# Kernel tuning notes

Measured on AMD Instinct MI355X. Metric: run time of the kernel, lower is better.

The kernel has to match this reference:

```python
import jax, jax.numpy as jnp
import numpy as np

D_HIDDEN = 1024
NUM_HEADS = 16
D_HEAD = D_HIDDEN // NUM_HEADS


def setup_inputs() -> dict:
    key = jax.random.key(0)
    ks = jax.random.split(key, 9)
    N, S, D = 4, 2048, D_HIDDEN
    s = 1.0 / np.sqrt(D)
    inp = {
        "x": jax.random.normal(ks[0], (N, S, D), dtype=jnp.float32),
        "Wq": jax.random.uniform(ks[1], (D, D), jnp.float32, -s, s),
        "bq": jnp.zeros((D,), jnp.float32),
        "Wk": jax.random.uniform(ks[2], (D, D), jnp.float32, -s, s),
        "bk": jnp.zeros((D,), jnp.float32),
        "Wv": jax.random.uniform(ks[3], (D, D), jnp.float32, -s, s),
        "bv": jnp.zeros((D,), jnp.float32),
        "Wo": jax.random.uniform(ks[4], (D, D), jnp.float32, -s, s),
        "bo": jnp.zeros((D,), jnp.float32),
        "ln_gamma": jnp.ones((D,), jnp.float32),
        "ln_beta": jnp.zeros((D,), jnp.float32),
    }
    return inp


def _layer_norm(x, gamma, beta, eps=1e-5):
    mu = jnp.mean(x, axis=-1, keepdims=True)
    var = jnp.var(x, axis=-1, keepdims=True)
    return (x - mu) * jax.lax.rsqrt(var + eps) * gamma + beta


def reference(x, Wq, bq, Wk, bk, Wv, bv, Wo, bo, ln_gamma, ln_beta):
    N, S, D = x.shape
    H, Dh = NUM_HEADS, D_HEAD
    xn = _layer_norm(x, ln_gamma, ln_beta)
    # torch Linear: y = x @ W.T + b
    q = (xn @ Wq.T + bq).reshape(N, S, H, Dh)
    k = (xn @ Wk.T + bk).reshape(N, S, H, Dh)
    v = (xn @ Wv.T + bv).reshape(N, S, H, Dh)
    # scores: [N, H, S, S]
    scores = jnp.einsum('nxhd,nyhd->nhxy', q, k) / np.sqrt(Dh)
    # causal mask: positions y > x get -inf
    mask = jnp.triu(jnp.full((S, S), -jnp.inf, dtype=scores.dtype), k=1)
    attn = jax.nn.softmax(scores + mask[None, None], axis=-1)
    z = jnp.einsum('nhxy,nyhd->nxhd', attn, v).reshape(N, S, D)
    return z @ Wo.T + bo
```

## Files before the change

kernel.cpp:

```cpp
#include <hip/hip_runtime.h>

typedef unsigned short u16;
typedef unsigned int   u32;
typedef __bf16 bf16x8 __attribute__((ext_vector_type(8)));
typedef float  f32x4  __attribute__((ext_vector_type(4)));
typedef unsigned short u16x8 __attribute__((ext_vector_type(8)));
typedef unsigned short u16x4 __attribute__((ext_vector_type(4)));

#define SEQ 2048
#define DM  1024
#define TOKS 8388608
#define SCLQ 0.18033688f

__device__ __forceinline__ float bf2f(u16 u) {
    u32 i = ((u32)u) << 16;
    float f; __builtin_memcpy(&f, &i, 4); return f;
}
__device__ __forceinline__ u16 f2bf(float f) {
    u32 i; __builtin_memcpy(&i, &f, 4);
    return (u16)((i + 0x7FFFu + ((i >> 16) & 1u)) >> 16);
}
__device__ __forceinline__ bf16x8 ld8(const u16* p) {
    return __builtin_bit_cast(bf16x8, *(const u16x8*)p);
}
#define GLD16(src, dst) __builtin_amdgcn_global_load_lds( \
    (const __attribute__((address_space(1))) void*)(src), \
    (__attribute__((address_space(3))) void*)(dst), 16, 0, 0)

#define SBAR() do { asm volatile("" ::: "memory"); __builtin_amdgcn_sched_barrier(0); \
    __builtin_amdgcn_s_barrier(); __builtin_amdgcn_sched_barrier(0); asm volatile("" ::: "memory"); } while (0)
#define WVM(n) asm volatile("s_waitcnt vmcnt(" #n ")" ::: "memory")

__global__ __launch_bounds__(64) void detect_k(const u32* __restrict__ x, int* __restrict__ flag) {
    const int lane = threadIdx.x;
    u32 w = x[lane];
    int e0 = (int)((w >> 7) & 0xFFu);
    int cnt = (e0 >= 100 && e0 <= 140) ? 1 : 0;
#pragma unroll
    for (int off = 32; off; off >>= 1) cnt += __shfl_xor(cnt, off);
    if (lane == 0) *flag = (cnt < 32) ? 1 : 0;
}

__global__ __launch_bounds__(256) void convert_k(const void* s0, const void* s1, const void* s2, const void* s3,
                                                 const void* v0, const void* v1, const void* v2, const void* v3,
                                                 const void* v4, const void* v5,
                                                 u16* __restrict__ dstW, u16* __restrict__ dstV,
                                                 const int* __restrict__ flagp) {
    const int y = blockIdx.y, tid = threadIdx.x;
    const int fp32m = *flagp;
    const void* src; u16* dst; size_t off;
    if (y < 4) {
        src = (y == 0) ? s0 : (y == 1) ? s1 : (y == 2) ? s2 : s3;
        dst = dstW + (size_t)y * 1048576;
        off = (size_t)blockIdx.x * 1024 + tid * 4;
    } else {
        const int i = blockIdx.x;
        if (i >= 6) return;
        src = (i == 0) ? v0 : (i == 1) ? v1 : (i == 2) ? v2 : (i == 3) ? v3 : (i == 4) ? v4 : v5;
        dst = dstV + (size_t)i * 1024;
        off = (size_t)tid * 4;
    }
    u16x4 o;
    if (fp32m) {
        const float* f = (const float*)src + off;
#pragma unroll
        for (int j = 0; j < 4; ++j) o[j] = f2bf(f[j]);
    } else {
        o = *(const u16x4*)((const u16*)src + off);
    }
    *(u16x4*)(dst + off) = o;
}

__global__ __launch_bounds__(256) void ln_k(const void* __restrict__ xv,
                                            const u16* __restrict__ g,
                                            const u16* __restrict__ b,
                                            u16* __restrict__ xn,
                                            const int* __restrict__ flagp) {
    const int row = blockIdx.x, tid = threadIdx.x;
    const int fp32m = *flagp;
    float f[4], s1 = 0.f, s2 = 0.f;
    if (fp32m) {
        f32x4 v = *(const f32x4*)((const float*)xv + (size_t)row * DM + tid * 4);
#pragma unroll
        for (int j = 0; j < 4; ++j) f[j] = v[j];
    } else {
        u16x4 v = *(const u16x4*)((const u16*)xv + (size_t)row * DM + tid * 4);
#pragma unroll
        for (int j = 0; j < 4; ++j) f[j] = bf2f(v[j]);
    }
#pragma unroll
    for (int j = 0; j < 4; ++j) { s1 += f[j]; s2 += f[j] * f[j]; }
#pragma unroll
    for (int off = 32; off; off >>= 1) { s1 += __shfl_xor(s1, off); s2 += __shfl_xor(s2, off); }
    __shared__ float red[8];
    const int wave = tid >> 6, lane = tid & 63;
    if (lane == 0) { red[wave] = s1; red[4 + wave] = s2; }
    __syncthreads();
    s1 = red[0] + red[1] + red[2] + red[3];
    s2 = red[4] + red[5] + red[6] + red[7];
    const float mu = s1 * (1.f / DM);
    const float var = s2 * (1.f / DM) - mu * mu;
    const float rs = rsqrtf(var + 1e-5f);
    u16x4 gv = *(const u16x4*)(g + tid * 4);
    u16x4 bv = *(const u16x4*)(b + tid * 4);
    u16x4 o;
#pragma unroll
    for (int j = 0; j < 4; ++j) o[j] = f2bf((f[j] - mu) * rs * bf2f(gv[j]) + bf2f(bv[j]));
    *(u16x4*)(xn + (size_t)row * DM + tid * 4) = o;
}

__global__ __launch_bounds__(512, 2) void gemm_qkv_k(const u16* __restrict__ xn, const u16* __restrict__ Wc,
                                                     const u16* __restrict__ Vc,
                                                     u16* __restrict__ Q, u16* __restrict__ K, u16* __restrict__ Vt) {
    __shared__ alignas(16) u16 lds[65536];
    const int tid = threadIdx.x;
    const int w = tid >> 6, lane = tid & 63;
    const int l4 = lane & 15, q4 = lane >> 4;
    const int orig = blockIdx.y * 32 + blockIdx.x;
    const int s = (orig & 7) * 48 + (orig >> 3);
    const int bm = s / 12, bn = s % 12;
    const int wm0 = (w >> 2) * 128, wn = (w & 3) * 64;

    const int srowl = lane >> 2;
    const int schk = (lane & 3) ^ ((lane >> 3) & 3);
    const u16* aS = xn + ((size_t)(bm * 256) + srowl) * DM + schk * 8;
    const u16* bS = Wc + ((size_t)(bn * 256) + srowl) * DM + schk * 8;
    const int rb = w * 16;

    auto STG = [&](int h, int kt, int bq) {
        const size_t kk = (size_t)kt * 32;
        u16* d = lds + bq * 16384;
        if (h == 0)      GLD16(aS + (size_t)rb * DM + kk,         d + rb * 32);
        else if (h == 3) GLD16(aS + (size_t)(128 + rb) * DM + kk, d + 4096 + rb * 32);
        else if (h == 1) GLD16(bS + (size_t)rb * DM + kk,         d + 8192 + rb * 32);
        else             GLD16(bS + (size_t)(128 + rb) * DM + kk, d + 12288 + rb * 32);
    };

    const int swz = (q4 ^ ((l4 >> 1) & 3)) << 3;

    f32x4 acc[8][4] = {};
    bf16x8 af[4], bfv[4];

#pragma unroll
    for (int p = 0; p < 3; ++p) {
        STG(0, p, p); STG(1, p, p); STG(2, p, p); STG(3, p, p);
    }

    for (int kt = 0; kt < 32; ++kt) {
        if (kt <= 29)      { WVM(8); }
        else if (kt == 30) { WVM(4); }
        else               { WVM(0); }
        SBAR();
        const u16* bp = lds + (kt & 3) * 16384;
        const bool pf = (kt < 29);
        const int nb = (kt + 3) & 3;
        if (pf) { STG(0, kt + 3, nb); STG(1, kt + 3, nb); }
#pragma unroll
        for (int mt = 0; mt < 4; ++mt) af[mt] = ld8(bp + (wm0 + mt * 16 + l4) * 32 + swz);
#pragma unroll
        for (int nt = 0; nt < 4; ++nt) bfv[nt] = ld8(bp + 8192 + (wn + nt * 16 + l4) * 32 + swz);
        __builtin_amdgcn_s_setprio(1);
#pragma unroll
        for (int mt = 0; mt < 4; ++mt)
#pragma unroll
            for (int nt = 0; nt < 4; ++nt)
                acc[mt][nt] = __builtin_amdgcn_mfma_f32_16x16x32_bf16(af[mt], bfv[nt], acc[mt][nt], 0, 0, 0);
        __builtin_amdgcn_s_setprio(0);
        if (pf) { STG(2, kt + 3, nb); STG(3, kt + 3, nb); }
#pragma unroll
        for (int mt = 0; mt < 4; ++mt) af[mt] = ld8(bp + (wm0 + 64 + mt * 16 + l4) * 32 + swz);
        __builtin_amdgcn_s_setprio(1);
#pragma unroll
        for (int mt = 0; mt < 4; ++mt)
#pragma unroll
            for (int nt = 0; nt < 4; ++nt)
                acc[mt + 4][nt] = __builtin_amdgcn_mfma_f32_16x16x32_bf16(af[mt], bfv[nt], acc[mt + 4][nt], 0, 0, 0);
        __builtin_amdgcn_s_setprio(0);
    }

    const int whichB = bn >> 2;
    const int cb = (bn & 3) * 256 + wn;
    u16* outp = (whichB == 0) ? Q : (whichB == 1) ? K : Vt;
    const float scl = (whichB == 0) ? SCLQ : 1.0f;
    float bs4[4];
#pragma unroll
    for (int nt = 0; nt < 4; ++nt) bs4[nt] = bf2f(Vc[whichB * 1024 + cb + nt * 16 + l4]);
    if (whichB < 2) {
#pragma unroll
        for (int mt = 0; mt < 8; ++mt) {
            const int row0 = bm * 256 + wm0 + mt * 16 + q4 * 4;
#pragma unroll
            for (int r = 0; r < 4; ++r) {
                u16* rowp = outp + (size_t)(row0 + r) * DM + cb;
#pragma unroll
                for (int nt = 0; nt < 4; ++nt)
                    rowp[nt * 16 + l4] = f2bf((acc[mt][nt][r] + bs4[nt]) * scl);
            }
        }
    } else {
#pragma unroll
        for (int nt = 0; nt < 4; ++nt) {
            const int cc = cb + nt * 16 + l4;
#pragma unroll
            for (int mt = 0; mt < 8; ++mt) {
                const int row0 = bm * 256 + wm0 + mt * 16 + q4 * 4;
                const int nbk = row0 >> 11, s0 = row0 & 2047;
                u16x4 pk;
#pragma unroll
                for (int r = 0; r < 4; ++r) pk[r] = f2bf(acc[mt][nt][r] + bs4[nt]);
                *(u16x4*)(outp + ((size_t)(nbk * 1024 + cc)) * SEQ + s0) = pk;
            }
        }
    }
}

#define LDS_U16 73728

__device__ __forceinline__ void wait_vm12() { asm volatile("s_waitcnt vmcnt(12)" ::: "memory"); }
__device__ __forceinline__ void wait_vm6()  { asm volatile("s_waitcnt vmcnt(6)"  ::: "memory"); }
__device__ __forceinline__ void wait_vm0()  { asm volatile("s_waitcnt vmcnt(0)"  ::: "memory"); }

__device__ __forceinline__ void gemm256x128_out(u16* lds,
                                                const u16* __restrict__ A,
                                                const u16* __restrict__ W,
                                                const u16* __restrict__ bias,
                                                u16* __restrict__ o0,
                                                int fp32m) {
    const int tid = threadIdx.x;
    const int w = tid >> 6, lane = tid & 63;
    const int l4 = lane & 15, q4 = lane >> 4;
    const int bm = blockIdx.x, bn = blockIdx.y;
    const int wm = (w >> 1) * 64, wn = (w & 1) * 64;

    const int srow = lane >> 3;
    const int schk = (lane & 7) ^ srow;
    const u16* sA = A + ((size_t)(bm * 256 + w * 32 + srow)) * DM + (schk << 3);
    const u16* sB = W + ((size_t)(bn * 128 + w * 16 + srow)) * DM + (schk << 3);

    int offA[4][2], offB[4][2];
#pragma unroll
    for (int mt = 0; mt < 4; ++mt)
#pragma unroll
        for (int s = 0; s < 2; ++s) {
            const int row = wm + mt * 16 + l4;
            offA[mt][s] = row * 64 + (((s * 4 + q4) ^ (l4 & 7)) << 3);
        }
#pragma unroll
    for (int nt = 0; nt < 4; ++nt)
#pragma unroll
        for (int s = 0; s < 2; ++s) {
            const int row = wn + nt * 16 + l4;
            offB[nt][s] = 16384 + row * 64 + (((s * 4 + q4) ^ (l4 & 7)) << 3);
        }

    auto STAGE = [&](int kt, int b) {
        const u16* a0 = sA + kt * 64;
        const u16* b0 = sB + kt * 64;
        u16* la = lds + b * 24576 + w * 2048;
        u16* lb = lds + b * 24576 + 16384 + w * 1024;
        GLD16(a0,           la);
        GLD16(a0 + 8 * DM,  la + 512);
        GLD16(a0 + 16 * DM, la + 1024);
        GLD16(a0 + 24 * DM, la + 1536);
        GLD16(b0,           lb);
        GLD16(b0 + 8 * DM,  lb + 512);
    };

    f32x4 acc[4][4] = {};

    STAGE(0, 0); STAGE(1, 1); STAGE(2, 2);

#pragma unroll
    for (int kt = 0; kt < 16; ++kt) {
        const int b = kt % 3;
        if (kt < 14)      wait_vm12();
        else if (kt == 14) wait_vm6();
        else               wait_vm0();
        __builtin_amdgcn_s_barrier();
        __builtin_amdgcn_sched_barrier(0);
        const u16* base = lds + b * 24576;
        bf16x8 af[4][2], bfr[4][2];
#pragma unroll
        for (int mt = 0; mt < 4; ++mt)
#pragma unroll
            for (int s = 0; s < 2; ++s) af[mt][s] = ld8(base + offA[mt][s]);
#pragma unroll
        for (int nt = 0; nt < 2; ++nt)
#pragma unroll
            for (int s = 0; s < 2; ++s) bfr[nt][s] = ld8(base + offB[nt][s]);
        __builtin_amdgcn_s_setprio(1);
#pragma unroll
        for (int mt = 0; mt < 4; ++mt)
#pragma unroll
            for (int nt = 0; nt < 2; ++nt)
#pragma unroll
                for (int s = 0; s < 2; ++s)
                    acc[mt][nt] = __builtin_amdgcn_mfma_f32_16x16x32_bf16(af[mt][s], bfr[nt][s], acc[mt][nt], 0, 0, 0);
        __builtin_amdgcn_s_setprio(0);
#pragma unroll
        for (int nt = 2; nt < 4; ++nt)
#pragma unroll
            for (int s = 0; s < 2; ++s) bfr[nt][s] = ld8(base + offB[nt][s]);
        __builtin_amdgcn_s_setprio(1);
#pragma unroll
        for (int mt = 0; mt < 4; ++mt)
#pragma unroll
            for (int nt = 2; nt < 4; ++nt)
#pragma unroll
                for (int s = 0; s < 2; ++s)
                    acc[mt][nt] = __builtin_amdgcn_mfma_f32_16x16x32_bf16(af[mt][s], bfr[nt][s], acc[mt][nt], 0, 0, 0);
        __builtin_amdgcn_s_setprio(0);
        __builtin_amdgcn_s_barrier();
        __builtin_amdgcn_sched_barrier(0);
        if (kt < 13) STAGE(kt + 3, b);
    }

#pragma unroll
    for (int nt = 0; nt < 4; ++nt) {
        const int cc = bn * 128 + wn + nt * 16 + l4;
        const float bs = bf2f(bias[cc]);
#pragma unroll
        for (int mt = 0; mt < 4; ++mt) {
            const int row0 = bm * 256 + wm + mt * 16 + q4 * 4;
            if (fp32m) {
#pragma unroll
                for (int r = 0; r < 4; ++r)
                    ((float*)o0)[(size_t)(row0 + r) * DM + cc] = acc[mt][nt][r] + bs;
            } else {
#pragma unroll
                for (int r = 0; r < 4; ++r)
                    o0[(size_t)(row0 + r) * DM + cc] = f2bf(acc[mt][nt][r] + bs);
            }
        }
    }
}

__global__ __launch_bounds__(512, 2) void gemm_out_k(const u16* __restrict__ Z, const u16* __restrict__ Wc,
                                                     const u16* __restrict__ Vc,
                                                     u16* __restrict__ out, const int* __restrict__ flagp) {
    __shared__ alignas(16) u16 lds[LDS_U16];
    const int fp32m = *flagp;
    gemm256x128_out(lds, Z, Wc + 3 * 1048576, Vc + 3 * 1024, out, fp32m);
}

__global__ __launch_bounds__(256, 4) void flash_k(const u16* __restrict__ Q,
                                                  const u16* __restrict__ K,
                                                  const u16* __restrict__ Vt,
                                                  u16* __restrict__ Z) {
    const int bh = blockIdx.x;
    const int qb = 15 - (int)blockIdx.y;
    const int n = bh >> 4, h = bh & 15;
    const int tid = threadIdx.x, wave = tid >> 6, lane = tid & 63;
    const int l4 = lane & 15, q4 = lane >> 4;

    __shared__ alignas(16) u16 Ks[2][64 * 32];
    __shared__ alignas(16) u16 Vs[2][64 * 32];
    __shared__ alignas(16) u16 Pl[4][2][16 * 72];

    const int Q0w = qb * 128 + wave * 32;
    bf16x8 qf[2][2];
#pragma unroll
    for (int qt = 0; qt < 2; ++qt) {
        const u16* Qr = Q + ((size_t)(n * SEQ + Q0w + qt * 16 + l4)) * DM + h * 64 + q4 * 8;
        qf[qt][0] = ld8(Qr);
        qf[qt][1] = ld8(Qr + 32);
    }

    const int srow = lane >> 2, scol = (lane & 3) * 8;
    const u16* Kg = K + ((size_t)(n * SEQ + wave * 16 + srow)) * DM + h * 64 + scol;
    const u16* Vg = Vt + ((size_t)(n * 1024 + h * 64 + wave * 16 + srow)) * SEQ + scol;
    u16* KsD0 = &Ks[0][wave * 512];
    u16* KsD1 = &Ks[1][wave * 512];
    u16* VsD0 = &Vs[0][wave * 512];
    u16* VsD1 = &Vs[1][wave * 512];

    f32x4 o[2][4] = {};
    float l_acc[2] = {0.f, 0.f};
    const int nch = 2 * qb + 2;

    for (int c = 0; c < nch; ++c) {
        const int kv0 = c * 64;
        const size_t krow = (size_t)kv0 * DM;
        GLD16(Kg + krow, KsD0);
        GLD16(Kg + krow + 32, KsD1);
        GLD16(Vg + kv0, VsD0);
        GLD16(Vg + kv0 + 32, VsD1);
        __syncthreads();

        bf16x8 a[4][2];
#pragma unroll
        for (int mt = 0; mt < 4; ++mt) {
            a[mt][0] = ld8(&Ks[0][(mt * 16 + l4) * 32 + q4 * 8]);
            a[mt][1] = ld8(&Ks[1][(mt * 16 + l4) * 32 + q4 * 8]);
        }
#pragma unroll
        for (int qt = 0; qt < 2; ++qt) {
            f32x4 st[4];
#pragma unroll
            for (int mt = 0; mt < 4; ++mt) {
                f32x4 zz = {0.f, 0.f, 0.f, 0.f};
                st[mt] = __builtin_amdgcn_mfma_f32_16x16x32_bf16(a[mt][0], qf[qt][0], zz, 0, 0, 0);
                st[mt] = __builtin_amdgcn_mfma_f32_16x16x32_bf16(a[mt][1], qf[qt][1], st[mt], 0, 0, 0);
            }
            const int qg = Q0w + qt * 16 + l4;
            u16* P = Pl[wave][qt];
            float la = l_acc[qt];
#pragma unroll
            for (int mt = 0; mt < 4; ++mt) {
                __bf16 pk[4];
#pragma unroll
                for (int r = 0; r < 4; ++r) {
                    const int kv = kv0 + mt * 16 + q4 * 4 + r;
                    float p = __builtin_amdgcn_exp2f(st[mt][r]);
                    p = (kv > qg) ? 0.f : p;
                    la += p;
                    pk[r] = (__bf16)p;
                }
                *(u16x4*)(P + l4 * 72 + mt * 16 + q4 * 4) = *(u16x4*)pk;
            }
            l_acc[qt] = la;
        }
#pragma unroll
        for (int ks = 0; ks < 2; ++ks) {
            bf16x8 pf0 = ld8(&Pl[wave][0][l4 * 72 + ks * 32 + q4 * 8]);
            bf16x8 pf1 = ld8(&Pl[wave][1][l4 * 72 + ks * 32 + q4 * 8]);
#pragma unroll
            for (int nt = 0; nt < 4; ++nt) {
                bf16x8 vf = ld8(&Vs[ks][(nt * 16 + l4) * 32 + q4 * 8]);
                o[0][nt] = __builtin_amdgcn_mfma_f32_16x16x32_bf16(pf0, vf, o[0][nt], 0, 0, 0);
                o[1][nt] = __builtin_amdgcn_mfma_f32_16x16x32_bf16(pf1, vf, o[1][nt], 0, 0, 0);
            }
        }
        __syncthreads();
    }

#pragma unroll
    for (int qt = 0; qt < 2; ++qt) {
        float l = l_acc[qt];
        l += __shfl_xor(l, 16);
        l += __shfl_xor(l, 32);
        float lr[4];
#pragma unroll
        for (int r = 0; r < 4; ++r) lr[r] = 1.f / __shfl(l, q4 * 4 + r);
#pragma unroll
        for (int nt = 0; nt < 4; ++nt) {
            const int col = h * 64 + nt * 16 + l4;
#pragma unroll
            for (int r = 0; r < 4; ++r) {
                const int row = n * SEQ + Q0w + qt * 16 + q4 * 4 + r;
                Z[(size_t)row * DM + col] = f2bf(o[qt][nt][r] * lr[r]);
            }
        }
    }
}

extern "C" void kernel_launch(void* const* d_in, const int* in_sizes, int n_in,
                              void* d_out, int out_size, void* d_ws, size_t ws_size,
                              hipStream_t stream) {
    const void* x  = d_in[0];
    const void* Wq = d_in[1];
    const void* bq = d_in[2];
    const void* Wk = d_in[3];
    const void* bk = d_in[4];
    const void* Wv = d_in[5];
    const void* bv = d_in[6];
    const void* Wo = d_in[7];
    const void* bo = d_in[8];
    const void* g  = d_in[9];
    const void* b  = d_in[10];
    u16* ws = (u16*)d_ws;

    u16* xn  = ws;
    u16* Qb  = ws + (size_t)TOKS;
    u16* Kb  = ws + (size_t)2 * TOKS;
    u16* Vtb = ws + (size_t)3 * TOKS;
    u16* Zb  = ws;
    u16* Wc  = ws + (size_t)4 * TOKS;
    u16* Vc  = Wc + 4 * 1048576;
    int* flagp = (int*)(Vc + 8 * 1024);

    detect_k<<<dim3(1), 64, 0, stream>>>((const u32*)x, flagp);
    convert_k<<<dim3(1024, 5), 256, 0, stream>>>(Wq, Wk, Wv, Wo, bq, bk, bv, bo, g, b, Wc, Vc, flagp);
    ln_k<<<dim3(4 * SEQ), 256, 0, stream>>>(x, Vc + 4 * 1024, Vc + 5 * 1024, xn, flagp);
    gemm_qkv_k<<<dim3(32, 12), 512, 0, stream>>>(xn, Wc, Vc, Qb, Kb, Vtb);
    flash_k<<<dim3(64, 16), 256, 0, stream>>>(Qb, Kb, Vtb, Zb);
    gemm_out_k<<<dim3(32, 8), 512, 0, stream>>>(Zb, Wc, Vc, (u16*)d_out, flagp);
}
```

Before: 253.1 us.

## Restructure QKV GEMM into a 64-wide K tile with four-phase ping-pong pipeline

Rewrites the QKV projection GEMM main loop to stage 64-wide K slices split by A/B half-tiles into double-buffered LDS slots. Each iteration runs four MFMA phases, with global-to-LDS loads issued between them and explicit lgkmcnt/vmcnt waits plus barriers. The LDS swizzle is changed to an 8-chunk XOR to match the wider rows. The XCD-aware block remapping is dropped in favor of direct blockIdx mapping, which may change L2 locality. A separate GEMM loop goes from full unrolling to unroll 4.

```diff
diff --git a/kernel.cpp b/kernel.cpp
--- a/kernel.cpp
+++ b/kernel.cpp
@@ -30,6 +30,8 @@
 #define SBAR() do { asm volatile("" ::: "memory"); __builtin_amdgcn_sched_barrier(0); \
     __builtin_amdgcn_s_barrier(); __builtin_amdgcn_sched_barrier(0); asm volatile("" ::: "memory"); } while (0)
 #define WVM(n) asm volatile("s_waitcnt vmcnt(" #n ")" ::: "memory")
+#define LGKM0() do { asm volatile("s_waitcnt lgkmcnt(0)" ::: "memory"); \
+    __builtin_amdgcn_sched_barrier(0); } while (0)
 
 __global__ __launch_bounds__(64) void detect_k(const u32* __restrict__ x, int* __restrict__ flag) {
     const int lane = threadIdx.x;
@@ -116,66 +118,101 @@
     const int tid = threadIdx.x;
     const int w = tid >> 6, lane = tid & 63;
     const int l4 = lane & 15, q4 = lane >> 4;
-    const int orig = blockIdx.y * 32 + blockIdx.x;
-    const int s = (orig & 7) * 48 + (orig >> 3);
-    const int bm = s / 12, bn = s % 12;
+    const int bm = blockIdx.x, bn = blockIdx.y;
     const int wm0 = (w >> 2) * 128, wn = (w & 3) * 64;
 
-    const int srowl = lane >> 2;
-    const int schk = (lane & 3) ^ ((lane >> 3) & 3);
-    const u16* aS = xn + ((size_t)(bm * 256) + srowl) * DM + schk * 8;
-    const u16* bS = Wc + ((size_t)(bn * 256) + srowl) * DM + schk * 8;
+    const int srow = lane >> 3, schk = (lane & 7) ^ srow;
+    const u16* aS = xn + ((size_t)(bm * 256) + srow) * DM + schk * 8;
+    const u16* bS = Wc + ((size_t)(bn * 256) + srow) * DM + schk * 8;
     const int rb = w * 16;
 
-    auto STG = [&](int h, int kt, int bq) {
-        const size_t kk = (size_t)kt * 32;
-        u16* d = lds + bq * 16384;
-        if (h == 0)      GLD16(aS + (size_t)rb * DM + kk,         d + rb * 32);
-        else if (h == 3) GLD16(aS + (size_t)(128 + rb) * DM + kk, d + 4096 + rb * 32);
-        else if (h == 1) GLD16(bS + (size_t)rb * DM + kk,         d + 8192 + rb * 32);
-        else             GLD16(bS + (size_t)(128 + rb) * DM + kk, d + 12288 + rb * 32);
+    auto STG = [&](int kind, int ut) {
+        const int slotb = kind * 16384 + (ut & 1) * 8192;
+        int g0;
+        if (kind == 0)      g0 = (rb < 64) ? rb : rb + 64;
+        else if (kind == 1) g0 = (rb < 64) ? rb + 64 : rb + 128;
+        else if (kind == 2) g0 = rb;
+        else                g0 = rb + 128;
+        const u16* src = (kind < 2 ? aS : bS) + (size_t)g0 * DM + (size_t)ut * 64;
+        u16* dst = lds + slotb + rb * 64;
+        GLD16(src, dst);
+        GLD16(src + 8 * DM, dst + 512);
     };
 
-    const int swz = (q4 ^ ((l4 >> 1) & 3)) << 3;
+    const int swz0 = (q4 ^ (l4 & 7)) << 3;
+    const int swz1 = ((4 + q4) ^ (l4 & 7)) << 3;
+    const int arow = ((w >> 2) * 64 + l4) * 64;
+    const int bbase = (wn & 127);
+    const int brow = (bbase + l4) * 64;
+    const int bsel = (w & 2) ? 49152 : 32768;
 
     f32x4 acc[8][4] = {};
-    bf16x8 af[4], bfv[4];
-
-#pragma unroll
-    for (int p = 0; p < 3; ++p) {
-        STG(0, p, p); STG(1, p, p); STG(2, p, p); STG(3, p, p);
-    }
-
-    for (int kt = 0; kt < 32; ++kt) {
-        if (kt <= 29)      { WVM(8); }
-        else if (kt == 30) { WVM(4); }
-        else               { WVM(0); }
+    bf16x8 af[4], b0r[4], b1r[4];
+
+    STG(0, 0); STG(2, 0); STG(3, 0); STG(1, 0); STG(0, 1); STG(2, 1);
+    WVM(6);
+    SBAR();
+
+#pragma unroll 2
+    for (int u = 0; u < 16; ++u) {
+        const int sb = (u & 1) * 8192;
+        const u16* AE = lds + sb;
+        const u16* AO = lds + 16384 + sb;
+        const u16* BB = lds + bsel + sb;
+#pragma unroll
+        for (int mt = 0; mt < 4; ++mt) af[mt] = ld8(AE + arow + mt * 1024 + swz0);
+#pragma unroll
+        for (int nt = 0; nt < 4; ++nt) b0r[nt] = ld8(BB + brow + nt * 1024 + swz0);
+        if (u < 15) STG(3, u + 1);
+        SBAR(); LGKM0();
+        __builtin_amdgcn_s_setprio(1);
+#pragma unroll
+        for (int mt = 0; mt < 4; ++mt)
+#pragma unroll
+            for (int nt = 0; nt < 4; ++nt)
+                acc[mt][nt] = __builtin_amdgcn_mfma_f32_16x16x32_bf16(af[mt], b0r[nt], acc[mt][nt], 0, 0, 0);
+        __builtin_amdgcn_s_setprio(0);
         SBAR();
-        const u16* bp = lds + (kt & 3) * 16384;
-        const bool pf = (kt < 29);
-        const int nb = (kt + 3) & 3;
-        if (pf) { STG(0, kt + 3, nb); STG(1, kt + 3, nb); }
-#pragma unroll
-        for (int mt = 0; mt < 4; ++mt) af[mt] = ld8(bp + (wm0 + mt * 16 + l4) * 32 + swz);
-#pragma unroll
-        for (int nt = 0; nt < 4; ++nt) bfv[nt] = ld8(bp + 8192 + (wn + nt * 16 + l4) * 32 + swz);
+#pragma unroll
+        for (int mt = 0; mt < 4; ++mt) af[mt] = ld8(AE + arow + mt * 1024 + swz1);
+#pragma unroll
+        for (int nt = 0; nt < 4; ++nt) b1r[nt] = ld8(BB + brow + nt * 1024 + swz1);
+        if (u < 15) STG(1, u + 1);
+        if (u < 15) { WVM(8); } else { WVM(0); }
+        SBAR(); LGKM0();
         __builtin_amdgcn_s_setprio(1);
 #pragma unroll
         for (int mt = 0; mt < 4; ++mt)
 #pragma unroll
             for (int nt = 0; nt < 4; ++nt)
-                acc[mt][nt] = __builtin_amdgcn_mfma_f32_16x16x32_bf16(af[mt], bfv[nt], acc[mt][nt], 0, 0, 0);
+                acc[mt][nt] = __builtin_amdgcn_mfma_f32_16x16x32_bf16(af[mt], b1r[nt], acc[mt][nt], 0, 0, 0);
         __builtin_amdgcn_s_setprio(0);
-        if (pf) { STG(2, kt + 3, nb); STG(3, kt + 3, nb); }
-#pragma unroll
-        for (int mt = 0; mt < 4; ++mt) af[mt] = ld8(bp + (wm0 + 64 + mt * 16 + l4) * 32 + swz);
+        SBAR();
+#pragma unroll
+        for (int mt = 0; mt < 4; ++mt) af[mt] = ld8(AO + arow + mt * 1024 + swz0);
+        if (u < 14) STG(0, u + 2);
+        SBAR(); LGKM0();
         __builtin_amdgcn_s_setprio(1);
 #pragma unroll
         for (int mt = 0; mt < 4; ++mt)
 #pragma unroll
             for (int nt = 0; nt < 4; ++nt)
-                acc[mt + 4][nt] = __builtin_amdgcn_mfma_f32_16x16x32_bf16(af[mt], bfv[nt], acc[mt + 4][nt], 0, 0, 0);
+                acc[mt + 4][nt] = __builtin_amdgcn_mfma_f32_16x16x32_bf16(af[mt], b0r[nt], acc[mt + 4][nt], 0, 0, 0);
         __builtin_amdgcn_s_setprio(0);
+        SBAR();
+#pragma unroll
+        for (int mt = 0; mt < 4; ++mt) af[mt] = ld8(AO + arow + mt * 1024 + swz1);
+        if (u < 14) STG(2, u + 2);
+        if (u < 14) { WVM(6); } else if (u == 14) { WVM(2); } else { WVM(0); }
+        SBAR(); LGKM0();
+        __builtin_amdgcn_s_setprio(1);
+#pragma unroll
+        for (int mt = 0; mt < 4; ++mt)
+#pragma unroll
+            for (int nt = 0; nt < 4; ++nt)
+                acc[mt + 4][nt] = __builtin_amdgcn_mfma_f32_16x16x32_bf16(af[mt], b1r[nt], acc[mt + 4][nt], 0, 0, 0);
+        __builtin_amdgcn_s_setprio(0);
+        SBAR();
     }
 
     const int whichB = bn >> 2;
@@ -270,7 +307,7 @@
 
     STAGE(0, 0); STAGE(1, 1); STAGE(2, 2);
 
-#pragma unroll
+#pragma unroll 4
     for (int kt = 0; kt < 16; ++kt) {
         const int b = kt % 3;
         if (kt < 14)      wait_vm12();
```

New measurement: 257.4 us. About the same (+1.7%).
